# Optimization experiments

Measured on AMD Instinct MI355X. Metric: run time of the kernel, lower is better.

The kernel has to match this reference:

```python
import jax, jax.numpy as jnp
import numpy as np
from jax import lax

DIM = 192
HEADS = 8
B, H, W = 2, 256, 256
EPS = 1e-12  # F.normalize default eps


def conv1x1(x, w):
    # x: [b, ci, h, w], w: [co, ci]
    return jnp.einsum('oi,bihw->bohw', w, x)


def dwconv3x3(x, w):
    # depthwise 3x3, SAME padding; w: [c, 1, 3, 3]
    c = x.shape[1]
    return lax.conv_general_dilated(
        x, w, window_strides=(1, 1), padding='SAME',
        dimension_numbers=('NCHW', 'OIHW', 'NCHW'),
        feature_group_count=c)


def l2norm(x):
    # F.normalize over last axis
    n = jnp.sqrt(jnp.sum(x * x, axis=-1, keepdims=True))
    return x / jnp.maximum(n, EPS)


def setup_inputs() -> dict:
    key = jax.random.key(0)
    ks = jax.random.split(key, 8)
    s = 0.02
    return {
        'x': jax.random.normal(ks[0], (B, DIM, H, W), jnp.float32),
        'x_ref': jax.random.normal(ks[1], (B, DIM, H, W), jnp.float32),
        'wq': jax.random.normal(ks[2], (DIM, DIM), jnp.float32) * s,
        'wq_dw': jax.random.normal(ks[3], (DIM, 1, 3, 3), jnp.float32) * s,
        'wkv': jax.random.normal(ks[4], (2 * DIM, DIM), jnp.float32) * s,
        'wkv_dw': jax.random.normal(ks[5], (2 * DIM, 1, 3, 3), jnp.float32) * s,
        'wproj': jax.random.normal(ks[6], (DIM, DIM), jnp.float32) * s,
        'temperature': jnp.ones((HEADS, 1, 1), jnp.float32),
    }


def reference(x, x_ref, wq, wq_dw, wkv, wkv_dw, wproj, temperature):
    b, c, h, w = x.shape
    ch = c // HEADS  # channels per head
    hw = h * w

    q = dwconv3x3(conv1x1(x, wq), wq_dw)            # [b, c, h, w]
    kv = dwconv3x3(conv1x1(x_ref, wkv), wkv_dw)      # [b, 2c, h, w]
    k, v = jnp.split(kv, 2, axis=1)

    q = q.reshape(b, HEADS, ch, hw)
    k = k.reshape(b, HEADS, ch, hw)
    v = v.reshape(b, HEADS, ch, hw)

    q = l2norm(q)
    k = l2norm(k)

    # channel-wise attention: [b, head, ch, ch]
    attn = jnp.einsum('bhcn,bhdn->bhcd', q, k) * temperature
    attn = jax.nn.softmax(attn, axis=-1)
    out = jnp.einsum('bhcd,bhdn->bhcn', attn, v)     # [b, head, ch, hw]

    out = out.reshape(b, c, h, w)
    out = conv1x1(out, wproj)
    return out
```

## Files before the change

kernel.cpp:

```cpp
#include <hip/hip_runtime.h>
#include <hip/hip_bf16.h>

#define B_ 2
#define C_ 192
#define HEADS_ 8
#define CH_ 24
#define H_ 256
#define W_ 256
#define HW_ 65536


using bf16x8 = __attribute__((ext_vector_type(8))) __bf16;
using f32x4  = __attribute__((ext_vector_type(4))) float;

__device__ __forceinline__ float b2f_us(unsigned short u) {
    return __uint_as_float(((unsigned)u) << 16);
}
__device__ __forceinline__ unsigned short f2bf(float f) {
    union { __hip_bfloat16 b; unsigned short u; } cv;
    cv.b = __float2bfloat16(f);
    return cv.u;
}

__global__ __launch_bounds__(256) void convert_w(
    const float* __restrict__ wq, const float* __restrict__ wkv,
    unsigned short* __restrict__ wqbf, unsigned short* __restrict__ wkvbf)
{
    int i = blockIdx.x * 256 + threadIdx.x;
    const float* src; unsigned short* dst; int qd;
    if (i < 9216) { src = wq;  dst = wqbf;  qd = i; }
    else          { src = wkv; dst = wkvbf; qd = i - 9216; }
    float4 v = *(const float4*)(src + (size_t)qd * 4);
    ushort4 u;
    u.x = f2bf(v.x); u.y = f2bf(v.y); u.z = f2bf(v.z); u.w = f2bf(v.w);
    *(ushort4*)(dst + (size_t)qd * 4) = u;
}

template<int NT, bool B_F32, bool OUT_F32>
__global__ __launch_bounds__(256) void gemm_mfma(
    const unsigned short* __restrict__ A, long a_bstride,
    const void* __restrict__ Bv, void* __restrict__ Outv, int outC)
{
    constexpr int S = 6 * NT;
    const int nb0 = blockIdx.x * (64 * NT);
    const int mt = blockIdx.y;
    const int b  = blockIdx.z;
    const int t  = threadIdx.x;

    __shared__ unsigned short Bl[3][64 * 40];

    const unsigned short* Ab = A + (size_t)b * a_bstride + (size_t)mt * 192 * 192;
    const int w = t >> 6, l = t & 63, li = l & 15, q = l >> 4;
    const int p0 = (t & 15) * 4;
    const int kp = t >> 4;

    const float* Bf = (const float*)Bv + (size_t)b * 192 * HW_;
    const unsigned short* Bh = (const unsigned short*)Bv + (size_t)b * 192 * HW_;

    float4  rf[2][2];
    ushort4 rh[2][2];
    bf16x8  af[2][3];

    auto LOADB = [&](int c, int set) {
        const int ti = c / 6, kc = c % 6;
        const size_t off = (size_t)(kc * 32 + kp * 2) * HW_ + nb0 + ti * 64 + p0;
        if constexpr (B_F32) {
            rf[set][0] = *(const float4*)(Bf + off);
            rf[set][1] = *(const float4*)(Bf + off + HW_);
        } else {
            rh[set][0] = *(const ushort4*)(Bh + off);
            rh[set][1] = *(const ushort4*)(Bh + off + HW_);
        }
    };
    auto CVTW = [&](int c, int set) {
        unsigned pk2[4];
        if constexpr (B_F32) {
            pk2[0] = (unsigned)f2bf(rf[set][0].x) | ((unsigned)f2bf(rf[set][1].x) << 16);
            pk2[1] = (unsigned)f2bf(rf[set][0].y) | ((unsigned)f2bf(rf[set][1].y) << 16);
            pk2[2] = (unsigned)f2bf(rf[set][0].z) | ((unsigned)f2bf(rf[set][1].z) << 16);
            pk2[3] = (unsigned)f2bf(rf[set][0].w) | ((unsigned)f2bf(rf[set][1].w) << 16);
        } else {
            pk2[0] = (unsigned)rh[set][0].x | ((unsigned)rh[set][1].x << 16);
            pk2[1] = (unsigned)rh[set][0].y | ((unsigned)rh[set][1].y << 16);
            pk2[2] = (unsigned)rh[set][0].z | ((unsigned)rh[set][1].z << 16);
            pk2[3] = (unsigned)rh[set][0].w | ((unsigned)rh[set][1].w << 16);
        }
        unsigned short* dst = &Bl[c % 3][kp * 2];
#pragma unroll
        for (int c4 = 0; c4 < 4; c4++) {
            int p = p0 + c4;
            int rB = ((p & 3) << 4) | (p >> 2);
            *(unsigned int*)&dst[rB * 40] = pk2[c4];
        }
    };
    auto AFLOAD = [&](int kc, int set) {
#pragma unroll
        for (int mi = 0; mi < 3; mi++)
            af[set][mi] = *(const bf16x8*)(Ab + (size_t)(w * 48 + mi * 16 + li) * 192
                                              + kc * 32 + q * 8);
    };

    f32x4 acc[3][4];
#pragma unroll
    for (int mi = 0; mi < 3; mi++)
#pragma unroll
        for (int ni = 0; ni < 4; ni++)
            acc[mi][ni] = (f32x4){0.f, 0.f, 0.f, 0.f};

    LOADB(0, 0);
    LOADB(1, 1);
    AFLOAD(0, 0);
    CVTW(0, 0);
    LOADB(2, 0);

#pragma unroll
    for (int s = 0; s < S; s++) {
        if (s + 1 < S) {
            CVTW(s + 1, (s + 1) & 1);
            AFLOAD((s + 1) % 6, (s + 1) & 1);
        }
        if (s + 3 < S) LOADB(s + 3, (s + 1) & 1);
        asm volatile("s_waitcnt lgkmcnt(0)" ::: "memory");
        __builtin_amdgcn_s_barrier();

        bf16x8 bfr[4];
#pragma unroll
        for (int ni = 0; ni < 4; ni++)
            bfr[ni] = *(const bf16x8*)&Bl[s % 3][(ni * 16 + li) * 40 + q * 8];
#pragma unroll
        for (int mi = 0; mi < 3; mi++)
#pragma unroll
            for (int ni = 0; ni < 4; ni++)
                acc[mi][ni] = __builtin_amdgcn_mfma_f32_16x16x32_bf16(
                    af[s & 1][mi], bfr[ni], acc[mi][ni], 0, 0, 0);

        if ((s % 6) == 5) {
            const int nb = nb0 + (s / 6) * 64;
            if (OUT_F32) {
                float* Ob = (float*)Outv + ((size_t)b * outC + (size_t)mt * 192) * HW_;
#pragma unroll
                for (int mi = 0; mi < 3; mi++)
#pragma unroll
                    for (int r = 0; r < 4; r++) {
                        int o = w * 48 + mi * 16 + q * 4 + r;
                        float4 vv;
                        vv.x = acc[mi][0][r]; vv.y = acc[mi][1][r];
                        vv.z = acc[mi][2][r]; vv.w = acc[mi][3][r];
                        *(float4*)(Ob + (size_t)o * HW_ + nb + 4 * li) = vv;
                    }
            } else {
                unsigned short* Ob = (unsigned short*)Outv + ((size_t)b * outC + (size_t)mt * 192) * HW_;
#pragma unroll
                for (int mi = 0; mi < 3; mi++)
#pragma unroll
                    for (int r = 0; r < 4; r++) {
                        int o = w * 48 + mi * 16 + q * 4 + r;
                        ushort4 u;
                        u.x = f2bf(acc[mi][0][r]); u.y = f2bf(acc[mi][1][r]);
                        u.z = f2bf(acc[mi][2][r]); u.w = f2bf(acc[mi][3][r]);
                        *(ushort4*)(Ob + (size_t)o * HW_ + nb + 4 * li) = u;
                    }
            }
#pragma unroll
            for (int mi = 0; mi < 3; mi++)
#pragma unroll
                for (int ni = 0; ni < 4; ni++)
                    acc[mi][ni] = (f32x4){0.f, 0.f, 0.f, 0.f};
        }
    }
}

#define VYG 4
__global__ __launch_bounds__(256) void dwconv_v(
    const __hip_bfloat16* __restrict__ tmpKV, const float* __restrict__ wkv_dw,
    __hip_bfloat16* __restrict__ V)
{
    const int y0 = blockIdx.x * VYG, cg = blockIdx.y, b = blockIdx.z;
    const int t = threadIdx.x;
    const int c = cg * 32 + (t >> 3);
    const int x0 = (t & 7) * 32;
    const unsigned short* base =
        (const unsigned short*)(tmpKV + ((size_t)b * 2 * C_ + C_ + c) * HW_);
    const float* wp = wkv_dw + (size_t)(C_ + c) * 9;
    float wgt[9];
#pragma unroll
    for (int i = 0; i < 9; i++) wgt[i] = wp[i];

    for (int yi = 0; yi < VYG; yi++) {
        const int y = y0 + yi;
        float o[32];
#pragma unroll
        for (int i = 0; i < 32; i++) o[i] = 0.f;

#pragma unroll
        for (int dy = -1; dy <= 1; dy++) {
            int yy = y + dy;
            if ((unsigned)yy >= 256u) continue;
            const unsigned short* r = base + yy * W_;
            float v[34];
            v[0]  = (x0 > 0) ? b2f_us(r[x0 - 1]) : 0.f;
            v[33] = (x0 + 32 < 256) ? b2f_us(r[x0 + 32]) : 0.f;
            const uint4* r4 = (const uint4*)(r + x0);
#pragma unroll
            for (int m = 0; m < 4; m++) {
                uint4 raw = r4[m];
                unsigned u;
                u = raw.x; v[1 + 8*m + 0] = __uint_as_float(u << 16); v[1 + 8*m + 1] = __uint_as_float(u & 0xffff0000u);
                u = raw.y; v[1 + 8*m + 2] = __uint_as_float(u << 16); v[1 + 8*m + 3] = __uint_as_float(u & 0xffff0000u);
                u = raw.z; v[1 + 8*m + 4] = __uint_as_float(u << 16); v[1 + 8*m + 5] = __uint_as_float(u & 0xffff0000u);
                u = raw.w; v[1 + 8*m + 6] = __uint_as_float(u << 16); v[1 + 8*m + 7] = __uint_as_float(u & 0xffff0000u);
            }
            float w0 = wgt[3 * (dy + 1) + 0];
            float w1 = wgt[3 * (dy + 1) + 1];
            float w2 = wgt[3 * (dy + 1) + 2];
#pragma unroll
            for (int i = 0; i < 32; i++)
                o[i] += v[i] * w0 + v[i + 1] * w1 + v[i + 2] * w2;
        }
        unsigned short* dst = (unsigned short*)V + ((size_t)b * C_ + c) * HW_ + y * W_ + x0;
#pragma unroll
        for (int m = 0; m < 4; m++) {
            uint4 pk;
            pk.x = (unsigned)f2bf(o[8*m + 0]) | ((unsigned)f2bf(o[8*m + 1]) << 16);
            pk.y = (unsigned)f2bf(o[8*m + 2]) | ((unsigned)f2bf(o[8*m + 3]) << 16);
            pk.z = (unsigned)f2bf(o[8*m + 4]) | ((unsigned)f2bf(o[8*m + 5]) << 16);
            pk.w = (unsigned)f2bf(o[8*m + 6]) | ((unsigned)f2bf(o[8*m + 7]) << 16);
            *(uint4*)(dst + 8 * m) = pk;
        }
    }
}

#define PADB 264
#define YG 4
__global__ __launch_bounds__(256) void dw_qk_gram(
    const __hip_bfloat16* __restrict__ tmpQ,
    const __hip_bfloat16* __restrict__ tmpKV,
    const float* __restrict__ wq_dw, const float* __restrict__ wkv_dw,
    float* __restrict__ G, float* __restrict__ sq, float* __restrict__ sk)
{
    const int y0 = blockIdx.x * YG, h = blockIdx.y, b = blockIdx.z;
    const int t = threadIdx.x;

    __shared__ unsigned short Qs[CH_ * PADB];
    __shared__ unsigned short Ks[CH_ * PADB];
    __shared__ float sqs[CH_], sks[CH_];

    if (t < CH_) { sqs[t] = 0.f; sks[t] = 0.f; }

    const int w = t >> 6, l = t & 63, li = l & 15, q = l >> 4;
    const int tr = w >> 1, tc = w & 1;
    int ar = tr * 16 + li; if (ar > 23) ar = 23;
    int br = tc * 16 + li; if (br > 23) br = 23;
    const unsigned short* arow = &Qs[ar * PADB];
    const unsigned short* brow = &Ks[br * PADB];
    f32x4 acc = (f32x4){0.f, 0.f, 0.f, 0.f};

    __syncthreads();

    for (int yi = 0; yi < YG; yi++) {
        const int y = y0 + yi;

        for (int u = t; u < 384; u += 256) {
            const int tens = (u >= 192);
            const int rem = u - tens * 192;
            const int c = rem >> 3;
            const int x0 = (rem & 7) * 32;
            const unsigned short* base = tens
                ? (const unsigned short*)(tmpKV + ((size_t)b * 2 * C_ + h * CH_ + c) * HW_)
                : (const unsigned short*)(tmpQ  + ((size_t)b * C_     + h * CH_ + c) * HW_);
            const float* wp = (tens ? wkv_dw : wq_dw) + (size_t)(h * CH_ + c) * 9;

            float o[32];
#pragma unroll
            for (int i = 0; i < 32; i++) o[i] = 0.f;

#pragma unroll
            for (int dy = -1; dy <= 1; dy++) {
                int yy = y + dy;
                if ((unsigned)yy >= 256u) continue;
                const unsigned short* r = base + yy * W_;
                float v[34];
                v[0]  = (x0 > 0) ? b2f_us(r[x0 - 1]) : 0.f;
                v[33] = (x0 + 32 < 256) ? b2f_us(r[x0 + 32]) : 0.f;
                const uint4* r4 = (const uint4*)(r + x0);
#pragma unroll
                for (int m = 0; m < 4; m++) {
                    uint4 raw = r4[m];
                    unsigned uu;
                    uu = raw.x; v[1 + 8*m + 0] = __uint_as_float(uu << 16); v[1 + 8*m + 1] = __uint_as_float(uu & 0xffff0000u);
                    uu = raw.y; v[1 + 8*m + 2] = __uint_as_float(uu << 16); v[1 + 8*m + 3] = __uint_as_float(uu & 0xffff0000u);
                    uu = raw.z; v[1 + 8*m + 4] = __uint_as_float(uu << 16); v[1 + 8*m + 5] = __uint_as_float(uu & 0xffff0000u);
                    uu = raw.w; v[1 + 8*m + 6] = __uint_as_float(uu << 16); v[1 + 8*m + 7] = __uint_as_float(uu & 0xffff0000u);
                }
                float w0 = wp[3 * (dy + 1) + 0];
                float w1 = wp[3 * (dy + 1) + 1];
                float w2 = wp[3 * (dy + 1) + 2];
#pragma unroll
                for (int i = 0; i < 32; i++)
                    o[i] += v[i] * w0 + v[i + 1] * w1 + v[i + 2] * w2;
            }

            float s = 0.f;
#pragma unroll
            for (int i = 0; i < 32; i++) s += o[i] * o[i];
            atomicAdd(tens ? &sks[c] : &sqs[c], s);

            unsigned short* dst = (tens ? Ks : Qs) + c * PADB + x0;
#pragma unroll
            for (int m = 0; m < 4; m++) {
                uint4 pk;
                pk.x = (unsigned)f2bf(o[8*m + 0]) | ((unsigned)f2bf(o[8*m + 1]) << 16);
                pk.y = (unsigned)f2bf(o[8*m + 2]) | ((unsigned)f2bf(o[8*m + 3]) << 16);
                pk.z = (unsigned)f2bf(o[8*m + 4]) | ((unsigned)f2bf(o[8*m + 5]) << 16);
                pk.w = (unsigned)f2bf(o[8*m + 6]) | ((unsigned)f2bf(o[8*m + 7]) << 16);
                *(uint4*)(dst + 8 * m) = pk;
            }
        }
        __syncthreads();

#pragma unroll
        for (int ks = 0; ks < 8; ks++) {
            bf16x8 af = *(const bf16x8*)&arow[ks * 32 + q * 8];
            bf16x8 bf = *(const bf16x8*)&brow[ks * 32 + q * 8];
            acc = __builtin_amdgcn_mfma_f32_16x16x32_bf16(af, bf, acc, 0, 0, 0);
        }
        __syncthreads();
    }

    if (t < CH_) {
        atomicAdd(&sq[b * C_ + h * CH_ + t], sqs[t]);
        atomicAdd(&sk[b * C_ + h * CH_ + t], sks[t]);
    }

    float* Gb = G + (size_t)(b * HEADS_ + h) * CH_ * CH_;
    const int col = tc * 16 + li;
    if (col < CH_) {
#pragma unroll
        for (int r = 0; r < 4; r++) {
            int row = tr * 16 + q * 4 + r;
            if (row < CH_)
                atomicAdd(&Gb[row * CH_ + col], acc[r]);
        }
    }
}

__global__ __launch_bounds__(192) void softmax_proj(
    const float* __restrict__ G, const float* __restrict__ sq,
    const float* __restrict__ sk, const float* __restrict__ temperature,
    const float* __restrict__ wproj, unsigned short* __restrict__ Mbf)
{
    const int h = blockIdx.x, b = blockIdx.y, t = threadIdx.x;
    __shared__ float attn[CH_][CH_];
    __shared__ float rk[CH_];
    const float* Gb = G + (size_t)(b * HEADS_ + h) * CH_ * CH_;
    if (t < CH_)
        rk[t] = 1.f / fmaxf(sqrtf(sk[b * C_ + h * CH_ + t]), 1e-12f);
    __syncthreads();
    if (t < CH_) {
        float rq = 1.f / fmaxf(sqrtf(sq[b * C_ + h * CH_ + t]), 1e-12f);
        float tempv = temperature[h];
        float row[CH_];
        float mx = -1e30f;
        for (int d = 0; d < CH_; d++) {
            row[d] = Gb[t * CH_ + d] * rq * rk[d] * tempv;
            mx = fmaxf(mx, row[d]);
        }
        float s = 0.f;
        for (int d = 0; d < CH_; d++) { row[d] = __expf(row[d] - mx); s += row[d]; }
        float inv = 1.f / s;
        for (int d = 0; d < CH_; d++) attn[t][d] = row[d] * inv;
    }
    __syncthreads();
    const int o = t;
    float wrow[CH_];
    for (int c = 0; c < CH_; c++) wrow[c] = wproj[o * C_ + h * CH_ + c];
    for (int d = 0; d < CH_; d++) {
        float s = 0.f;
        for (int c = 0; c < CH_; c++) s += wrow[c] * attn[c][d];
        Mbf[((size_t)b * C_ + o) * C_ + h * CH_ + d] = f2bf(s);
    }
}

extern "C" void kernel_launch(void* const* d_in, const int* in_sizes, int n_in,
                              void* d_out, int out_size, void* d_ws, size_t ws_size,
                              hipStream_t stream)
{
    const float* x           = (const float*)d_in[0];
    const float* x_ref       = (const float*)d_in[1];
    const float* wq          = (const float*)d_in[2];
    const float* wq_dw       = (const float*)d_in[3];
    const float* wkv         = (const float*)d_in[4];
    const float* wkv_dw      = (const float*)d_in[5];
    const float* wproj       = (const float*)d_in[6];
    const float* temperature = (const float*)d_in[7];
    float* out = (float*)d_out;

    char* ws = (char*)d_ws;
    __hip_bfloat16* tmpQ  = (__hip_bfloat16*)(ws);
    __hip_bfloat16* tmpKV = (__hip_bfloat16*)(ws + 50331648);
    __hip_bfloat16* tmpV  = (__hip_bfloat16*)(ws);
    float* G  = (float*)(ws + 150994944);
    float* sq = (float*)(ws + 151031808);
    float* sk = (float*)(ws + 151033344);
    unsigned short* wqbf  = (unsigned short*)(ws + 151034880);
    unsigned short* wkvbf = (unsigned short*)(ws + 151108608);
    unsigned short* Mbf   = (unsigned short*)(ws + 151034880);

    hipMemsetAsync(G, 0, 36864 + 1536 + 1536, stream);

    convert_w<<<dim3(108), 256, 0, stream>>>(wq, wkv, wqbf, wkvbf);
    gemm_mfma<2, true, false><<<dim3(HW_ / 128, 1, B_), 256, 0, stream>>>(
        wqbf, 0, x, tmpQ, 192);
    gemm_mfma<2, true, false><<<dim3(HW_ / 128, 2, B_), 256, 0, stream>>>(
        wkvbf, 0, x_ref, tmpKV, 384);
    dw_qk_gram<<<dim3(H_ / YG, HEADS_, B_), 256, 0, stream>>>(
        tmpQ, tmpKV, wq_dw, wkv_dw, G, sq, sk);
    softmax_proj<<<dim3(HEADS_, B_), 192, 0, stream>>>(
        G, sq, sk, temperature, wproj, Mbf);
    dwconv_v<<<dim3(H_ / VYG, 6, B_), 256, 0, stream>>>(tmpKV, wkv_dw, tmpV);
    gemm_mfma<2, false, true><<<dim3(HW_ / 128, 1, B_), 256, 0, stream>>>(
        Mbf, 192 * 192, tmpV, out, 192);
}
```

Baseline: 445.7 us.

## Shrink GEMM tiles to one 64-column tile with double-buffered LDS pipeline

The 1x1-conv GEMM kernel drops the NT template so each block handles a single 64-pixel column tile, doubling the grid size. The LDS ring goes from triple to double buffering, with the barrier now placed after the MFMAs and the conversion of the next chunk. This aims for more blocks and less per-block register/LDS use, giving better latency hiding through occupancy. The cost is that each block reloads the 192x192 weight fragments twice as often, and the shallower prefetch may expose more global load latency.

```diff
diff --git a/kernel.cpp b/kernel.cpp
--- a/kernel.cpp
+++ b/kernel.cpp
@@ -36,18 +36,17 @@
     *(ushort4*)(dst + (size_t)qd * 4) = u;
 }
 
-template<int NT, bool B_F32, bool OUT_F32>
+template<bool B_F32, bool OUT_F32>
 __global__ __launch_bounds__(256) void gemm_mfma(
     const unsigned short* __restrict__ A, long a_bstride,
     const void* __restrict__ Bv, void* __restrict__ Outv, int outC)
 {
-    constexpr int S = 6 * NT;
-    const int nb0 = blockIdx.x * (64 * NT);
+    const int nb = blockIdx.x * 64;
     const int mt = blockIdx.y;
     const int b  = blockIdx.z;
     const int t  = threadIdx.x;
 
-    __shared__ unsigned short Bl[3][64 * 40];
+    __shared__ unsigned short Bl[2][64 * 40];
 
     const unsigned short* Ab = A + (size_t)b * a_bstride + (size_t)mt * 192 * 192;
     const int w = t >> 6, l = t & 63, li = l & 15, q = l >> 4;
@@ -61,9 +60,9 @@
     ushort4 rh[2][2];
     bf16x8  af[2][3];
 
-    auto LOADB = [&](int c, int set) {
-        const int ti = c / 6, kc = c % 6;
-        const size_t off = (size_t)(kc * 32 + kp * 2) * HW_ + nb0 + ti * 64 + p0;
+    auto LOADB = [&](int kc) {
+        const int set = kc & 1;
+        const size_t off = (size_t)(kc * 32 + kp * 2) * HW_ + nb + p0;
         if constexpr (B_F32) {
             rf[set][0] = *(const float4*)(Bf + off);
             rf[set][1] = *(const float4*)(Bf + off + HW_);
@@ -72,7 +71,8 @@
             rh[set][1] = *(const ushort4*)(Bh + off + HW_);
         }
     };
-    auto CVTW = [&](int c, int set) {
+    auto CVTW = [&](int kc) {
+        const int set = kc & 1;
         unsigned pk2[4];
         if constexpr (B_F32) {
             pk2[0] = (unsigned)f2bf(rf[set][0].x) | ((unsigned)f2bf(rf[set][1].x) << 16);
@@ -85,7 +85,7 @@
             pk2[2] = (unsigned)rh[set][0].z | ((unsigned)rh[set][1].z << 16);
             pk2[3] = (unsigned)rh[set][0].w | ((unsigned)rh[set][1].w << 16);
         }
-        unsigned short* dst = &Bl[c % 3][kp * 2];
+        unsigned short* dst = &Bl[set][kp * 2];
 #pragma unroll
         for (int c4 = 0; c4 < 4; c4++) {
             int p = p0 + c4;
@@ -93,11 +93,11 @@
             *(unsigned int*)&dst[rB * 40] = pk2[c4];
         }
     };
-    auto AFLOAD = [&](int kc, int set) {
+    auto AFLOAD = [&](int kc) {
 #pragma unroll
         for (int mi = 0; mi < 3; mi++)
-            af[set][mi] = *(const bf16x8*)(Ab + (size_t)(w * 48 + mi * 16 + li) * 192
-                                              + kc * 32 + q * 8);
+            af[kc & 1][mi] = *(const bf16x8*)(Ab + (size_t)(w * 48 + mi * 16 + li) * 192
+                                                 + kc * 32 + q * 8);
     };
 
     f32x4 acc[3][4];
@@ -107,66 +107,60 @@
         for (int ni = 0; ni < 4; ni++)
             acc[mi][ni] = (f32x4){0.f, 0.f, 0.f, 0.f};
 
-    LOADB(0, 0);
-    LOADB(1, 1);
-    AFLOAD(0, 0);
-    CVTW(0, 0);
-    LOADB(2, 0);
-
-#pragma unroll
-    for (int s = 0; s < S; s++) {
-        if (s + 1 < S) {
-            CVTW(s + 1, (s + 1) & 1);
-            AFLOAD((s + 1) % 6, (s + 1) & 1);
-        }
-        if (s + 3 < S) LOADB(s + 3, (s + 1) & 1);
-        asm volatile("s_waitcnt lgkmcnt(0)" ::: "memory");
-        __builtin_amdgcn_s_barrier();
+    LOADB(0);
+    LOADB(1);
+    AFLOAD(0);
+    CVTW(0);
+    asm volatile("s_waitcnt lgkmcnt(0)" ::: "memory");
+    __builtin_amdgcn_s_barrier();
+
+#pragma unroll
+    for (int c = 0; c < 6; c++) {
+        if (c + 1 < 6) AFLOAD(c + 1);
+        if (c + 2 < 6) LOADB(c + 2);
 
         bf16x8 bfr[4];
 #pragma unroll
         for (int ni = 0; ni < 4; ni++)
-            bfr[ni] = *(const bf16x8*)&Bl[s % 3][(ni * 16 + li) * 40 + q * 8];
+            bfr[ni] = *(const bf16x8*)&Bl[c & 1][(ni * 16 + li) * 40 + q * 8];
 #pragma unroll
         for (int mi = 0; mi < 3; mi++)
 #pragma unroll
             for (int ni = 0; ni < 4; ni++)
                 acc[mi][ni] = __builtin_amdgcn_mfma_f32_16x16x32_bf16(
-                    af[s & 1][mi], bfr[ni], acc[mi][ni], 0, 0, 0);
-
-        if ((s % 6) == 5) {
-            const int nb = nb0 + (s / 6) * 64;
-            if (OUT_F32) {
-                float* Ob = (float*)Outv + ((size_t)b * outC + (size_t)mt * 192) * HW_;
-#pragma unroll
-                for (int mi = 0; mi < 3; mi++)
-#pragma unroll
-                    for (int r = 0; r < 4; r++) {
-                        int o = w * 48 + mi * 16 + q * 4 + r;
-                        float4 vv;
-                        vv.x = acc[mi][0][r]; vv.y = acc[mi][1][r];
-                        vv.z = acc[mi][2][r]; vv.w = acc[mi][3][r];
-                        *(float4*)(Ob + (size_t)o * HW_ + nb + 4 * li) = vv;
-                    }
-            } else {
-                unsigned short* Ob = (unsigned short*)Outv + ((size_t)b * outC + (size_t)mt * 192) * HW_;
-#pragma unroll
-                for (int mi = 0; mi < 3; mi++)
-#pragma unroll
-                    for (int r = 0; r < 4; r++) {
-                        int o = w * 48 + mi * 16 + q * 4 + r;
-                        ushort4 u;
-                        u.x = f2bf(acc[mi][0][r]); u.y = f2bf(acc[mi][1][r]);
-                        u.z = f2bf(acc[mi][2][r]); u.w = f2bf(acc[mi][3][r]);
-                        *(ushort4*)(Ob + (size_t)o * HW_ + nb + 4 * li) = u;
-                    }
+                    af[c & 1][mi], bfr[ni], acc[mi][ni], 0, 0, 0);
+
+        if (c + 1 < 6) {
+            CVTW(c + 1);
+            asm volatile("s_waitcnt lgkmcnt(0)" ::: "memory");
+            __builtin_amdgcn_s_barrier();
+        }
+    }
+
+    if (OUT_F32) {
+        float* Ob = (float*)Outv + ((size_t)b * outC + (size_t)mt * 192) * HW_;
+#pragma unroll
+        for (int mi = 0; mi < 3; mi++)
+#pragma unroll
+            for (int r = 0; r < 4; r++) {
+                int o = w * 48 + mi * 16 + q * 4 + r;
+                float4 vv;
+                vv.x = acc[mi][0][r]; vv.y = acc[mi][1][r];
+                vv.z = acc[mi][2][r]; vv.w = acc[mi][3][r];
+                *(float4*)(Ob + (size_t)o * HW_ + nb + 4 * li) = vv;
             }
-#pragma unroll
-            for (int mi = 0; mi < 3; mi++)
-#pragma unroll
-                for (int ni = 0; ni < 4; ni++)
-                    acc[mi][ni] = (f32x4){0.f, 0.f, 0.f, 0.f};
-        }
+    } else {
+        unsigned short* Ob = (unsigned short*)Outv + ((size_t)b * outC + (size_t)mt * 192) * HW_;
+#pragma unroll
+        for (int mi = 0; mi < 3; mi++)
+#pragma unroll
+            for (int r = 0; r < 4; r++) {
+                int o = w * 48 + mi * 16 + q * 4 + r;
+                ushort4 u;
+                u.x = f2bf(acc[mi][0][r]); u.y = f2bf(acc[mi][1][r]);
+                u.z = f2bf(acc[mi][2][r]); u.w = f2bf(acc[mi][3][r]);
+                *(ushort4*)(Ob + (size_t)o * HW_ + nb + 4 * li) = u;
+            }
     }
 }
 
@@ -409,15 +403,15 @@
     hipMemsetAsync(G, 0, 36864 + 1536 + 1536, stream);
 
     convert_w<<<dim3(108), 256, 0, stream>>>(wq, wkv, wqbf, wkvbf);
-    gemm_mfma<2, true, false><<<dim3(HW_ / 128, 1, B_), 256, 0, stream>>>(
+    gemm_mfma<true, false><<<dim3(HW_ / 64, 1, B_), 256, 0, stream>>>(
         wqbf, 0, x, tmpQ, 192);
-    gemm_mfma<2, true, false><<<dim3(HW_ / 128, 2, B_), 256, 0, stream>>>(
+    gemm_mfma<true, false><<<dim3(HW_ / 64, 2, B_), 256, 0, stream>>>(
         wkvbf, 0, x_ref, tmpKV, 384);
     dw_qk_gram<<<dim3(H_ / YG, HEADS_, B_), 256, 0, stream>>>(
         tmpQ, tmpKV, wq_dw, wkv_dw, G, sq, sk);
     softmax_proj<<<dim3(HEADS_, B_), 192, 0, stream>>>(
         G, sq, sk, temperature, wproj, Mbf);
     dwconv_v<<<dim3(H_ / VYG, 6, B_), 256, 0, stream>>>(tmpKV, wkv_dw, tmpV);
-    gemm_mfma<2, false, true><<<dim3(HW_ / 128, 1, B_), 256, 0, stream>>>(
+    gemm_mfma<false, true><<<dim3(HW_ / 64, 1, B_), 256, 0, stream>>>(
         Mbf, 192 * 192, tmpV, out, 192);
 }
```

Result: no change. 444.3 us (-0.3%).
